# Kernel tuning notes

Measured on AMD Instinct MI355X. Metric: run time of the kernel, lower is better.

The kernel has to match this reference:

```python
import jax, jax.numpy as jnp
import numpy as np

N, E, F_IN = 100000, 1000000, 128
H, C = 4, 32
HC = H * C
D_DIR = 128
G = 250
HID, CLS = 128, 2
ALPHA = 0.5
NEG = 0.2  # LeakyReLU slope in GATv2


def setup_inputs() -> dict:
    key = jax.random.key(0)
    ks = jax.random.split(key, 16)
    p = lambda k, shape: 0.02 * jax.random.normal(k, shape, jnp.float32)
    return {
        "x": jax.random.normal(ks[0], (N, F_IN), jnp.float32),
        "edge_index": jax.random.randint(ks[1], (2, E), 0, N, dtype=jnp.int32),
        "edge_attr": jax.random.normal(ks[2], (E, 1), jnp.float32),
        "batch": jnp.sort(jax.random.randint(ks[3], (N,), 0, G, dtype=jnp.int32)),
        "dir_w_in": p(ks[4], (2, F_IN, D_DIR)),
        "dir_b_in": jnp.zeros((2, D_DIR), jnp.float32),
        "dir_w_out": p(ks[5], (2, F_IN, D_DIR)),
        "dir_b_out": jnp.zeros((2, D_DIR), jnp.float32),
        "gat_wl": p(ks[6], (F_IN, HC)),
        "gat_wr": p(ks[7], (F_IN, HC)),
        "gat_we": p(ks[8], (1, HC)),
        "gat_att": p(ks[9], (H, C)),
        "gat_b": jnp.zeros((HC,), jnp.float32),
        "w1": p(ks[10], (D_DIR + HC, HID)),
        "b1": jnp.zeros((HID,), jnp.float32),
        "w2": p(ks[11], (HID, CLS)),
        "b2": jnp.zeros((CLS,), jnp.float32),
    }


def _gcn(x, src, dst, W, b):
    # GCNConv with add_self_loops=False (forced by DirGNNConv), unit edge weights.
    deg = jnp.zeros((N,), x.dtype).at[dst].add(1.0)
    dinv = jnp.where(deg > 0, 1.0 / jnp.sqrt(jnp.maximum(deg, 1.0)), 0.0)
    norm = dinv[src] * dinv[dst]  # [E]
    h = x @ W  # [N, D]
    out = jnp.zeros((N, W.shape[1]), x.dtype).at[dst].add(norm[:, None] * h[src])
    return out + b


def _mean_pool(h, batch):
    cnt = jnp.zeros((G,), h.dtype).at[batch].add(1.0)
    s = jnp.zeros((G, h.shape[1]), h.dtype).at[batch].add(h)
    return s / jnp.maximum(cnt, 1.0)[:, None]


def _forward(x, edge_index, edge_attr, batch, dir_w_in, dir_b_in, dir_w_out, dir_b_out,
             gat_wl, gat_wr, gat_we, gat_att, gat_b, w1, b1, w2, b2):
    src, dst = edge_index[0], edge_index[1]
    # --- DirGNN branch: alpha * GCN(flipped edges) + (1-alpha) * GCN(edges), relu between ---
    h = x
    for i in range(2):
        x_in = _gcn(h, src, dst, dir_w_in[i], dir_b_in[i])
        x_out = _gcn(h, dst, src, dir_w_out[i], dir_b_out[i])
        h = jax.nn.relu(ALPHA * x_out + (1.0 - ALPHA) * x_in)
    x1 = _mean_pool(h, batch)  # [G, D_DIR]
    # --- GATv2 branch (self loops appended, edge_attr fill value 1.0) ---
    loop = jnp.arange(N, dtype=src.dtype)
    s2 = jnp.concatenate([src, loop])
    d2 = jnp.concatenate([dst, loop])
    ea = jnp.concatenate([edge_attr, jnp.ones((N, 1), edge_attr.dtype)], axis=0)
    gl = (x @ gat_wl).reshape(N, H, C)  # source transform
    gr = (x @ gat_wr).reshape(N, H, C)  # target transform
    ee = (ea @ gat_we).reshape(-1, H, C)
    e = jax.nn.leaky_relu(gl[s2] + gr[d2] + ee, NEG)  # [E+N, H, C]
    logits = jnp.einsum('ehc,hc->eh', e, gat_att)
    # segment softmax over incoming edges of each target node (self loops => nonempty)
    m = jnp.full((N, H), -jnp.inf, logits.dtype).at[d2].max(logits)
    ex = jnp.exp(logits - m[d2])
    denom = jnp.zeros((N, H), logits.dtype).at[d2].add(ex)
    att = ex / denom[d2]
    out2 = jnp.zeros((N, H, C), x.dtype).at[d2].add(att[:, :, None] * gl[s2])
    x2 = _mean_pool(out2.reshape(N, HC) + gat_b, batch)  # [G, HC]
    # --- head ---
    z = jnp.concatenate([x1, x2], axis=1)
    z = jax.nn.relu(z @ w1 + b1)
    return z @ w2 + b2  # [G, CLS]


def reference(x, edge_index, edge_attr, batch, dir_w_in, dir_b_in, dir_w_out, dir_b_out,
              gat_wl, gat_wr, gat_we, gat_att, gat_b, w1, b1, w2, b2):
    return _forward(x, edge_index, edge_attr, batch, dir_w_in, dir_b_in, dir_w_out, dir_b_out,
                    gat_wl, gat_wr, gat_we, gat_att, gat_b, w1, b1, w2, b2)
```

## Files before the change

kernel.cpp:

```cpp
#include <hip/hip_runtime.h>
#include <cstdint>

#define FDIM 128
#define PCH 64

static inline int cdiv(long long a, long long b) { return (int)((a + b - 1) / b); }

__global__ __launch_bounds__(256) void degi_kernel(const int* __restrict__ src,
                                                   const int* __restrict__ dst,
                                                   int* __restrict__ deg_in,
                                                   int* __restrict__ deg_out, int E) {
  int base = (blockIdx.x * 256 + threadIdx.x) * 2;
  if (base + 2 <= E) {
    int2 s2 = *(const int2*)(src + base);
    int2 d2 = *(const int2*)(dst + base);
    atomicAdd(&deg_in[d2.x], 1);
    atomicAdd(&deg_in[d2.y], 1);
    atomicAdd(&deg_out[s2.x], 1);
    atomicAdd(&deg_out[s2.y], 1);
  } else {
    for (int i = base; i < E; i++) {
      atomicAdd(&deg_in[dst[i]], 1);
      atomicAdd(&deg_out[src[i]], 1);
    }
  }
}

__global__ __launch_bounds__(256) void dinv2_kernel(const int* __restrict__ degs,
                                                    float* __restrict__ dinv, int n2) {
  int i = blockIdx.x * 256 + threadIdx.x;
  if (i < n2) {
    int v = degs[i];
    dinv[i] = v > 0 ? 1.0f / sqrtf((float)v) : 0.f;
  }
}

__global__ __launch_bounds__(256) void cnt_sorted(const int* __restrict__ batch,
                                                  float* __restrict__ cnt, int N, int G) {
  int g = blockIdx.x * 256 + threadIdx.x;
  if (g >= G) return;
  int lo = 0, hi = N;
  while (lo < hi) { int mid = (lo + hi) >> 1; if (batch[mid] < g) lo = mid + 1; else hi = mid; }
  int lo2 = lo, hi2 = N;
  while (lo2 < hi2) { int mid = (lo2 + hi2) >> 1; if (batch[mid] <= g) lo2 = mid + 1; else hi2 = mid; }
  cnt[g] = (float)(lo2 - lo);
}

__global__ __launch_bounds__(256) void scan1(const int* __restrict__ in, int* __restrict__ out,
                                             int* __restrict__ bsums, int n) {
  __shared__ int tmp[256];
  int t = threadIdx.x;
  int base = blockIdx.x * 1024 + t * 4;
  int a[4];
#pragma unroll
  for (int j = 0; j < 4; j++) a[j] = (base + j < n) ? in[base + j] : 0;
  int s = a[0] + a[1] + a[2] + a[3];
  tmp[t] = s;
  __syncthreads();
  for (int off = 1; off < 256; off <<= 1) {
    int v = (t >= off) ? tmp[t - off] : 0;
    __syncthreads();
    tmp[t] += v;
    __syncthreads();
  }
  int excl = tmp[t] - s;
  int run = excl;
#pragma unroll
  for (int j = 0; j < 4; j++) {
    if (base + j < n) out[base + j] = run;
    run += a[j];
  }
  if (t == 255) bsums[blockIdx.x] = tmp[255];
}

__global__ __launch_bounds__(256) void scan2(const int* __restrict__ bsums,
                                             int* __restrict__ boff, int nb) {
  __shared__ int tmp[256];
  int t = threadIdx.x;
  int s = (t < nb) ? bsums[t] : 0;
  tmp[t] = s;
  __syncthreads();
  for (int off = 1; off < 256; off <<= 1) {
    int v = (t >= off) ? tmp[t - off] : 0;
    __syncthreads();
    tmp[t] += v;
    __syncthreads();
  }
  if (t < nb) boff[t] = tmp[t] - s;
}

__global__ __launch_bounds__(256) void scan3(const int* __restrict__ scanned,
                                             const int* __restrict__ boff,
                                             int* __restrict__ rp_in, int* __restrict__ cur_in,
                                             int* __restrict__ rp_out, int* __restrict__ cur_out,
                                             int N, int E, int n2) {
  int i = blockIdx.x * 256 + threadIdx.x;
  if (i < n2) {
    int v = scanned[i] + boff[i >> 10];
    if (i < N) { rp_in[i] = v; cur_in[i] = v; }
    else { v -= E; rp_out[i - N] = v; cur_out[i - N] = v; }
  }
}

__global__ __launch_bounds__(256) void mm0_fill(const float* __restrict__ A,
                                                const float* __restrict__ W0,
                                                const float* __restrict__ W1,
                                                float* __restrict__ out0,
                                                float* __restrict__ out1, int nrows, int mmB,
                                                const int* __restrict__ src,
                                                const int* __restrict__ dst,
                                                const float* __restrict__ eattr,
                                                int* __restrict__ cur_in,
                                                int* __restrict__ cur_out,
                                                int2* __restrict__ csr_in,
                                                int* __restrict__ csr_out_dst, int E, int fillB) {
  __shared__ float As[64][128];
  __shared__ float Ws[64][64];
  int T = mmB + fillB;
  int bid = blockIdx.x;
  int tid = threadIdx.x;
  long long f0 = (long long)bid * fillB / T;
  long long f1 = (long long)(bid + 1) * fillB / T;

  if (f1 > f0) {
    int base = ((int)f0 * 256 + tid) * 4;
    if (base + 4 <= E) {
      int4 s4 = *(const int4*)(src + base);
      int4 d4 = *(const int4*)(dst + base);
      float4 e4 = *(const float4*)(eattr + base);
      int p0 = atomicAdd(&cur_in[d4.x], 1);
      int p1 = atomicAdd(&cur_in[d4.y], 1);
      int p2 = atomicAdd(&cur_in[d4.z], 1);
      int p3 = atomicAdd(&cur_in[d4.w], 1);
      int q0 = atomicAdd(&cur_out[s4.x], 1);
      int q1 = atomicAdd(&cur_out[s4.y], 1);
      int q2 = atomicAdd(&cur_out[s4.z], 1);
      int q3 = atomicAdd(&cur_out[s4.w], 1);
      csr_in[p0] = make_int2(s4.x, __float_as_int(e4.x));
      csr_in[p1] = make_int2(s4.y, __float_as_int(e4.y));
      csr_in[p2] = make_int2(s4.z, __float_as_int(e4.z));
      csr_in[p3] = make_int2(s4.w, __float_as_int(e4.w));
      csr_out_dst[q0] = d4.x;
      csr_out_dst[q1] = d4.y;
      csr_out_dst[q2] = d4.z;
      csr_out_dst[q3] = d4.w;
    } else {
      for (int i = base; i < E; i++) {
        int s = src[i], d = dst[i];
        int p = atomicAdd(&cur_in[d], 1);
        csr_in[p] = make_int2(s, __float_as_int(eattr[i]));
        int q = atomicAdd(&cur_out[s], 1);
        csr_out_dst[q] = d;
      }
    }
    return;
  }

  int mb = bid - (int)f0;
  int r0 = mb * 64;

#pragma unroll
  for (int i = 0; i < 8; i++) {
    int v = tid + 256 * i;
    int r = v >> 5, k4 = (v & 31) << 2;
    int row = r0 + r;
    float4 a;
    if (row < nrows) a = *(const float4*)(A + (size_t)row * FDIM + k4);
    else a = make_float4(0.f, 0.f, 0.f, 0.f);
    int swz = ((r >> 2) & 7) << 2;
    *(float4*)(&As[r][k4 ^ swz]) = a;
  }

  int tx = tid & 15, ty = tid >> 4;
  int rbase = ty * 4;
  int swz = (ty & 7) << 2;

  for (int p = 0; p < 4; p++) {
    const float* W = (p < 2) ? W0 : W1;
    float* out = (p < 2) ? out0 : out1;
    int cb = (p & 1) * 64;
    float acc[4][4] = {};

    for (int kh = 0; kh < 2; kh++) {
      __syncthreads();
#pragma unroll
      for (int i = 0; i < 4; i++) {
        int v = tid + 256 * i;
        int k = v >> 4, c4 = (v & 15) << 2;
        *(float4*)(&Ws[k][c4]) = *(const float4*)(W + (kh * 64 + k) * FDIM + cb + c4);
      }
      __syncthreads();

#pragma unroll 8
      for (int k = 0; k < 64; k++) {
        int kx = (kh * 64 + k) ^ swz;
        float a0 = As[rbase + 0][kx];
        float a1 = As[rbase + 1][kx];
        float a2 = As[rbase + 2][kx];
        float a3 = As[rbase + 3][kx];
        float4 w = *(float4*)(&Ws[k][tx * 4]);
        acc[0][0] += a0 * w.x; acc[0][1] += a0 * w.y; acc[0][2] += a0 * w.z; acc[0][3] += a0 * w.w;
        acc[1][0] += a1 * w.x; acc[1][1] += a1 * w.y; acc[1][2] += a1 * w.z; acc[1][3] += a1 * w.w;
        acc[2][0] += a2 * w.x; acc[2][1] += a2 * w.y; acc[2][2] += a2 * w.z; acc[2][3] += a2 * w.w;
        acc[3][0] += a3 * w.x; acc[3][1] += a3 * w.y; acc[3][2] += a3 * w.z; acc[3][3] += a3 * w.w;
      }
    }

#pragma unroll
    for (int rr = 0; rr < 4; rr++) {
      int row = r0 + rbase + rr;
      if (row < nrows) {
        float4 o = make_float4(acc[rr][0], acc[rr][1], acc[rr][2], acc[rr][3]);
        *(float4*)(out + (size_t)row * FDIM + cb + tx * 4) = o;
      }
    }
  }
}

__global__ __launch_bounds__(256) void mm128d(const float* __restrict__ A,
                                              const float* __restrict__ W0,
                                              const float* __restrict__ W1,
                                              float* __restrict__ out0,
                                              float* __restrict__ out1, int nrows) {
  __shared__ float As[64][128];
  __shared__ float Ws[64][64];
  int r0 = blockIdx.x * 64;
  int tid = threadIdx.x;

#pragma unroll
  for (int i = 0; i < 8; i++) {
    int v = tid + 256 * i;
    int r = v >> 5, k4 = (v & 31) << 2;
    int row = r0 + r;
    float4 a;
    if (row < nrows) a = *(const float4*)(A + (size_t)row * FDIM + k4);
    else a = make_float4(0.f, 0.f, 0.f, 0.f);
    int swz = ((r >> 2) & 7) << 2;
    *(float4*)(&As[r][k4 ^ swz]) = a;
  }

  int tx = tid & 15, ty = tid >> 4;
  int rbase = ty * 4;
  int swz = (ty & 7) << 2;

  for (int p = 0; p < 4; p++) {
    const float* W = (p < 2) ? W0 : W1;
    float* out = (p < 2) ? out0 : out1;
    int cb = (p & 1) * 64;
    float acc[4][4] = {};

    for (int kh = 0; kh < 2; kh++) {
      __syncthreads();
#pragma unroll
      for (int i = 0; i < 4; i++) {
        int v = tid + 256 * i;
        int k = v >> 4, c4 = (v & 15) << 2;
        *(float4*)(&Ws[k][c4]) = *(const float4*)(W + (kh * 64 + k) * FDIM + cb + c4);
      }
      __syncthreads();

#pragma unroll 8
      for (int k = 0; k < 64; k++) {
        int kx = (kh * 64 + k) ^ swz;
        float a0 = As[rbase + 0][kx];
        float a1 = As[rbase + 1][kx];
        float a2 = As[rbase + 2][kx];
        float a3 = As[rbase + 3][kx];
        float4 w = *(float4*)(&Ws[k][tx * 4]);
        acc[0][0] += a0 * w.x; acc[0][1] += a0 * w.y; acc[0][2] += a0 * w.z; acc[0][3] += a0 * w.w;
        acc[1][0] += a1 * w.x; acc[1][1] += a1 * w.y; acc[1][2] += a1 * w.z; acc[1][3] += a1 * w.w;
        acc[2][0] += a2 * w.x; acc[2][1] += a2 * w.y; acc[2][2] += a2 * w.z; acc[2][3] += a2 * w.w;
        acc[3][0] += a3 * w.x; acc[3][1] += a3 * w.y; acc[3][2] += a3 * w.z; acc[3][3] += a3 * w.w;
      }
    }

#pragma unroll
    for (int rr = 0; rr < 4; rr++) {
      int row = r0 + rbase + rr;
      if (row < nrows) {
        float4 o = make_float4(acc[rr][0], acc[rr][1], acc[rr][2], acc[rr][3]);
        *(float4*)(out + (size_t)row * FDIM + cb + tx * 4) = o;
      }
    }
  }
}

__global__ __launch_bounds__(128) void gcn_gather4(const float4* __restrict__ tin,
                                                   const float4* __restrict__ tout,
                                                   const int* __restrict__ rp_in,
                                                   const int* __restrict__ deg_in,
                                                   const int2* __restrict__ adj_in,
                                                   const int* __restrict__ rp_out,
                                                   const int* __restrict__ deg_out,
                                                   const int* __restrict__ adj_out,
                                                   const float* __restrict__ dinv_in,
                                                   const float* __restrict__ dinv_out,
                                                   const float* __restrict__ bin,
                                                   const float* __restrict__ bout,
                                                   float4* __restrict__ outp, int N) {
  int grp = threadIdx.x >> 5, lane = threadIdx.x & 31;
  int d = blockIdx.x * 4 + grp;
  if (d >= N) return;
  float wi = 0.5f * dinv_in[d], wo = 0.5f * dinv_out[d];
  float4 a0 = make_float4(0.f, 0.f, 0.f, 0.f);
  float4 a1 = a0, a2 = a0, a3 = a0;

  int p = rp_in[d], n1 = deg_in[d];
  int k = 0;
  for (; k + 4 <= n1; k += 4) {
    int s0 = adj_in[p + k].x, s1 = adj_in[p + k + 1].x, s2 = adj_in[p + k + 2].x, s3 = adj_in[p + k + 3].x;
    float w0 = wi * dinv_in[s0], w1 = wi * dinv_in[s1], w2 = wi * dinv_in[s2], w3 = wi * dinv_in[s3];
    float4 v0 = tin[(size_t)s0 * 32 + lane];
    float4 v1 = tin[(size_t)s1 * 32 + lane];
    float4 v2 = tin[(size_t)s2 * 32 + lane];
    float4 v3 = tin[(size_t)s3 * 32 + lane];
    a0.x += w0 * v0.x; a0.y += w0 * v0.y; a0.z += w0 * v0.z; a0.w += w0 * v0.w;
    a1.x += w1 * v1.x; a1.y += w1 * v1.y; a1.z += w1 * v1.z; a1.w += w1 * v1.w;
    a2.x += w2 * v2.x; a2.y += w2 * v2.y; a2.z += w2 * v2.z; a2.w += w2 * v2.w;
    a3.x += w3 * v3.x; a3.y += w3 * v3.y; a3.z += w3 * v3.z; a3.w += w3 * v3.w;
  }
  for (; k < n1; k++) {
    int s = adj_in[p + k].x;
    float w = wi * dinv_in[s];
    float4 v = tin[(size_t)s * 32 + lane];
    a0.x += w * v.x; a0.y += w * v.y; a0.z += w * v.z; a0.w += w * v.w;
  }

  int q = rp_out[d], n2 = deg_out[d];
  k = 0;
  for (; k + 4 <= n2; k += 4) {
    int s0 = adj_out[q + k], s1 = adj_out[q + k + 1], s2 = adj_out[q + k + 2], s3 = adj_out[q + k + 3];
    float w0 = wo * dinv_out[s0], w1 = wo * dinv_out[s1], w2 = wo * dinv_out[s2], w3 = wo * dinv_out[s3];
    float4 v0 = tout[(size_t)s0 * 32 + lane];
    float4 v1 = tout[(size_t)s1 * 32 + lane];
    float4 v2 = tout[(size_t)s2 * 32 + lane];
    float4 v3 = tout[(size_t)s3 * 32 + lane];
    a0.x += w0 * v0.x; a0.y += w0 * v0.y; a0.z += w0 * v0.z; a0.w += w0 * v0.w;
    a1.x += w1 * v1.x; a1.y += w1 * v1.y; a1.z += w1 * v1.z; a1.w += w1 * v1.w;
    a2.x += w2 * v2.x; a2.y += w2 * v2.y; a2.z += w2 * v2.z; a2.w += w2 * v2.w;
    a3.x += w3 * v3.x; a3.y += w3 * v3.y; a3.z += w3 * v3.z; a3.w += w3 * v3.w;
  }
  for (; k < n2; k++) {
    int s = adj_out[q + k];
    float w = wo * dinv_out[s];
    float4 v = tout[(size_t)s * 32 + lane];
    a0.x += w * v.x; a0.y += w * v.y; a0.z += w * v.z; a0.w += w * v.w;
  }

  float4 acc;
  acc.x = (a0.x + a1.x) + (a2.x + a3.x);
  acc.y = (a0.y + a1.y) + (a2.y + a3.y);
  acc.z = (a0.z + a1.z) + (a2.z + a3.z);
  acc.w = (a0.w + a1.w) + (a2.w + a3.w);

  const float4* b1 = (const float4*)bin;
  const float4* b2 = (const float4*)bout;
  float4 ba = b1[lane], bb = b2[lane];
  float4 o;
  o.x = acc.x + 0.5f * (ba.x + bb.x);
  o.y = acc.y + 0.5f * (ba.y + bb.y);
  o.z = acc.z + 0.5f * (ba.z + bb.z);
  o.w = acc.w + 0.5f * (ba.w + bb.w);
  o.x = o.x > 0.f ? o.x : 0.f;
  o.y = o.y > 0.f ? o.y : 0.f;
  o.z = o.z > 0.f ? o.z : 0.f;
  o.w = o.w > 0.f ? o.w : 0.f;
  outp[(size_t)d * 32 + lane] = o;
}

__global__ __launch_bounds__(128) void gat_fused2(const float4* __restrict__ gl,
                                                  const float4* __restrict__ gr,
                                                  const int* __restrict__ rp,
                                                  const int* __restrict__ deg,
                                                  const int2* __restrict__ adj,
                                                  const float* __restrict__ we,
                                                  const float* __restrict__ att,
                                                  const float* __restrict__ gatb,
                                                  float4* __restrict__ outp, int N) {
  int grp = threadIdx.x >> 5, lane = threadIdx.x & 31;
  int d = blockIdx.x * 4 + grp;
  if (d >= N) return;

  float4 grv = gr[(size_t)d * 32 + lane];
  float4 wev = ((const float4*)we)[lane];
  float4 atv = ((const float4*)att)[lane];

  int p = rp[d], n1 = deg[d];
  float m = -1e30f, den = 0.f;
  float4 o = make_float4(0.f, 0.f, 0.f, 0.f);

#define GAT_LOGIT(g4, ea, pv)                                                     \
  {                                                                               \
    float vx = g4.x + grv.x + (ea) * wev.x; vx = vx > 0.f ? vx : 0.2f * vx;       \
    float vy = g4.y + grv.y + (ea) * wev.y; vy = vy > 0.f ? vy : 0.2f * vy;       \
    float vz = g4.z + grv.z + (ea) * wev.z; vz = vz > 0.f ? vz : 0.2f * vz;       \
    float vw = g4.w + grv.w + (ea) * wev.w; vw = vw > 0.f ? vw : 0.2f * vw;       \
    pv = vx * atv.x + vy * atv.y + vz * atv.z + vw * atv.w;                       \
    pv += __shfl_xor(pv, 1);                                                      \
    pv += __shfl_xor(pv, 2);                                                      \
    pv += __shfl_xor(pv, 4);                                                      \
  }

#define GAT_UPDATE(g4, pv)                                                        \
  {                                                                               \
    float mn = fmaxf(m, pv);                                                      \
    float sc = expf(m - mn);                                                      \
    float w = expf(pv - mn);                                                      \
    den = den * sc + w;                                                           \
    o.x = o.x * sc + w * g4.x;                                                    \
    o.y = o.y * sc + w * g4.y;                                                    \
    o.z = o.z * sc + w * g4.z;                                                    \
    o.w = o.w * sc + w * g4.w;                                                    \
    m = mn;                                                                       \
  }

  int k = 0;
  for (; k + 2 <= n1; k += 2) {
    int2 e0 = adj[p + k], e1 = adj[p + k + 1];
    int s0 = e0.x, s1 = e1.x;
    float ea0 = __int_as_float(e0.y), ea1 = __int_as_float(e1.y);
    float4 g0 = gl[(size_t)s0 * 32 + lane];
    float4 g1 = gl[(size_t)s1 * 32 + lane];
    float pv0, pv1;
    GAT_LOGIT(g0, ea0, pv0);
    GAT_LOGIT(g1, ea1, pv1);
    GAT_UPDATE(g0, pv0);
    GAT_UPDATE(g1, pv1);
  }
  if (k < n1) {
    int2 e = adj[p + k];
    float ea = __int_as_float(e.y);
    float4 g = gl[(size_t)e.x * 32 + lane];
    float pv;
    GAT_LOGIT(g, ea, pv);
    GAT_UPDATE(g, pv);
  }
  {
    float4 g = gl[(size_t)d * 32 + lane];
    float pv;
    GAT_LOGIT(g, 1.0f, pv);
    GAT_UPDATE(g, pv);
  }
#undef GAT_LOGIT
#undef GAT_UPDATE

  float4 bb = ((const float4*)gatb)[lane];
  float4 r;
  r.x = o.x / den + bb.x;
  r.y = o.y / den + bb.y;
  r.z = o.z / den + bb.z;
  r.w = o.w / den + bb.w;
  outp[(size_t)d * 32 + lane] = r;
}

__global__ __launch_bounds__(128) void pool_kernel(const float* __restrict__ srcf,
                                                   const int* __restrict__ batch,
                                                   float* __restrict__ zb,
                                                   int colOff, int N) {
  __shared__ int sb[PCH];
  int c0 = blockIdx.x * PCH;
  int t = threadIdx.x;
  int nmax = N - c0; if (nmax > PCH) nmax = PCH;
  if (t < nmax) sb[t] = batch[c0 + t];
  __syncthreads();
  float run = 0.f;
  int gp = sb[0];
  for (int i = 0; i < nmax; i++) {
    int g = sb[i];
    if (g != gp) {
      atomicAdd(&zb[(size_t)gp * 256 + colOff + t], run);
      run = 0.f; gp = g;
    }
    run += srcf[(size_t)(c0 + i) * FDIM + t];
  }
  atomicAdd(&zb[(size_t)gp * 256 + colOff + t], run);
}

__global__ __launch_bounds__(128) void head_kernel(const float* __restrict__ zb,
                                                   const float* __restrict__ cnt,
                                                   const float* __restrict__ w1,
                                                   const float* __restrict__ b1,
                                                   const float* __restrict__ w2,
                                                   const float* __restrict__ b2,
                                                   float* __restrict__ out, int G) {
  __shared__ float z[256];
  __shared__ float y[128];
  int g = blockIdx.x, t = threadIdx.x;
  float c = cnt[g];
  float cm = c > 1.f ? c : 1.f;
  z[t]       = zb[(size_t)g * 256 + t] / cm;
  z[t + 128] = zb[(size_t)g * 256 + 128 + t] / cm;
  __syncthreads();
  float acc = b1[t];
  for (int k = 0; k < 256; k++) acc += z[k] * w1[k * 128 + t];
  y[t] = acc > 0.f ? acc : 0.f;
  __syncthreads();
  if (t < 2) {
    float o = b2[t];
    for (int j = 0; j < 128; j++) o += y[j] * w2[j * 2 + t];
    out[(size_t)g * 2 + t] = o;
  }
}

extern "C" void kernel_launch(void* const* d_in, const int* in_sizes, int n_in,
                              void* d_out, int out_size, void* d_ws, size_t ws_size,
                              hipStream_t stream) {
  const float* x     = (const float*)d_in[0];
  const int*   ei    = (const int*)d_in[1];
  const float* eattr = (const float*)d_in[2];
  const int*   batch = (const int*)d_in[3];
  const float* dwi   = (const float*)d_in[4];
  const float* dbi   = (const float*)d_in[5];
  const float* dwo   = (const float*)d_in[6];
  const float* dbo   = (const float*)d_in[7];
  const float* wl    = (const float*)d_in[8];
  const float* wr    = (const float*)d_in[9];
  const float* we    = (const float*)d_in[10];
  const float* att   = (const float*)d_in[11];
  const float* gatb  = (const float*)d_in[12];
  const float* w1    = (const float*)d_in[13];
  const float* b1    = (const float*)d_in[14];
  const float* w2    = (const float*)d_in[15];
  const float* b2    = (const float*)d_in[16];

  int N = in_sizes[0] / FDIM;
  int E = in_sizes[1] / 2;
  int G = out_size / 2;
  const int* src = ei;
  const int* dst = ei + E;

  float* ws = (float*)d_ws;
  size_t off = 0;
  float* A        = ws + off; off += (size_t)N * FDIM;
  float* B        = ws + off; off += (size_t)N * FDIM;
  float* C        = ws + off; off += (size_t)N * FDIM;
  float* dinv2    = ws + off; off += 2 * (size_t)N;
  int* deg2       = (int*)(ws + off); off += 2 * (size_t)N;
  int* rpt        = (int*)(ws + off); off += 2 * (size_t)N;
  int* rp_in      = (int*)(ws + off); off += (size_t)N;
  int* rp_out     = (int*)(ws + off); off += (size_t)N;
  int* cur_in     = (int*)(ws + off); off += (size_t)N;
  int* cur_out    = (int*)(ws + off); off += (size_t)N;
  int2* csr_in    = (int2*)(ws + off); off += 2 * (size_t)E;
  int* csr_out_dst= (int*)(ws + off); off += (size_t)E;
  int* bsums      = (int*)(ws + off); off += 256;
  int* boff       = (int*)(ws + off); off += 256;
  float* zb       = ws + off; off += (size_t)G * 256;
  float* cnt      = ws + off; off += (size_t)G;

  int* deg_in = deg2, *deg_out = deg2 + N;
  float* dinv_in = dinv2, *dinv_out = dinv2 + N;

  int n2 = 2 * N;
  int nb1 = cdiv(n2, 1024);

  hipMemsetAsync(deg2, 0, (size_t)n2 * sizeof(int), stream);
  degi_kernel<<<cdiv(E, 512), 256, 0, stream>>>(src, dst, deg_in, deg_out, E);
  dinv2_kernel<<<cdiv((long long)n2, 256), 256, 0, stream>>>(deg2, dinv2, n2);
  scan1<<<nb1, 256, 0, stream>>>(deg2, rpt, bsums, n2);
  scan2<<<1, 256, 0, stream>>>(bsums, boff, nb1);
  scan3<<<cdiv(n2, 256), 256, 0, stream>>>(rpt, boff, rp_in, cur_in, rp_out, cur_out, N, E, n2);

  hipMemsetAsync(zb, 0, (size_t)G * 256 * sizeof(float), stream);
  cnt_sorted<<<cdiv(G, 256), 256, 0, stream>>>(batch, cnt, N, G);

  int mmB = cdiv(N, 64);
  int fillB = cdiv(E, 1024);
  mm0_fill<<<mmB + fillB, 256, 0, stream>>>(x, dwi, dwo, B, C, N, mmB,
                                            src, dst, eattr, cur_in, cur_out,
                                            csr_in, csr_out_dst, E, fillB);

  gcn_gather4<<<cdiv(N, 4), 128, 0, stream>>>((const float4*)B, (const float4*)C,
                                              rp_in, deg_in, csr_in,
                                              rp_out, deg_out, csr_out_dst,
                                              dinv_in, dinv_out, dbi, dbo, (float4*)A, N);
  mm128d<<<mmB, 256, 0, stream>>>(A, dwi + 16384, dwo + 16384, B, C, N);
  gcn_gather4<<<cdiv(N, 4), 128, 0, stream>>>((const float4*)B, (const float4*)C,
                                              rp_in, deg_in, csr_in,
                                              rp_out, deg_out, csr_out_dst,
                                              dinv_in, dinv_out, dbi + 128, dbo + 128, (float4*)A, N);
  pool_kernel<<<cdiv(N, PCH), 128, 0, stream>>>(A, batch, zb, 0, N);

  mm128d<<<mmB, 256, 0, stream>>>(x, wl, wr, B, C, N);
  gat_fused2<<<cdiv(N, 4), 128, 0, stream>>>((const float4*)B, (const float4*)C,
                                             rp_in, deg_in, csr_in,
                                             we, att, gatb, (float4*)A, N);
  pool_kernel<<<cdiv(N, PCH), 128, 0, stream>>>(A, batch, zb, 128, N);

  head_kernel<<<G, 128, 0, stream>>>(zb, cnt, w1, b1, w2, b2, (float*)d_out, G);
}
```

Baseline: 1.082 ms.

## Fuse GAT matmul with degree count and fuse pooling into gather kernels

Moves the GAT input projection into the degree-counting kernel so the two run concurrently, using a fourth workspace buffer when space allows. GAT aggregation and the second GCN gather now atomically add their node results straight into the per-graph pooled sums, which removes the separate pool kernels and the round trip of the node feature matrix. The fused pooling relies on float atomics into a small per-graph array, which may contend and changes summation order. A fallback path keeps a three-buffer schedule when the workspace is too small.

After: 1.477 ms. 1.36x slower.

```diff
diff --git a/kernel.cpp b/kernel.cpp
--- a/kernel.cpp
+++ b/kernel.cpp
@@ -102,7 +102,257 @@
   }
 }
 
-__global__ __launch_bounds__(256) void mm0_fill(const float* __restrict__ A,
+
+__device__ __forceinline__ float4 gcn_node_val(int d, int lane,
+    const float4* __restrict__ tin, const float4* __restrict__ tout,
+    const int* __restrict__ rp_in, const int* __restrict__ deg_in, const int2* __restrict__ adj_in,
+    const int* __restrict__ rp_out, const int* __restrict__ deg_out, const int* __restrict__ adj_out,
+    const float* __restrict__ dinv_in, const float* __restrict__ dinv_out,
+    const float* __restrict__ bin, const float* __restrict__ bout) {
+  float wi = 0.5f * dinv_in[d], wo = 0.5f * dinv_out[d];
+  float4 a0 = make_float4(0.f, 0.f, 0.f, 0.f);
+  float4 a1 = a0, a2 = a0, a3 = a0;
+
+  int p = rp_in[d], n1 = deg_in[d];
+  int k = 0;
+  for (; k + 4 <= n1; k += 4) {
+    int s0 = adj_in[p + k].x, s1 = adj_in[p + k + 1].x, s2 = adj_in[p + k + 2].x, s3 = adj_in[p + k + 3].x;
+    float w0 = wi * dinv_in[s0], w1 = wi * dinv_in[s1], w2 = wi * dinv_in[s2], w3 = wi * dinv_in[s3];
+    float4 v0 = tin[(size_t)s0 * 32 + lane];
+    float4 v1 = tin[(size_t)s1 * 32 + lane];
+    float4 v2 = tin[(size_t)s2 * 32 + lane];
+    float4 v3 = tin[(size_t)s3 * 32 + lane];
+    a0.x += w0 * v0.x; a0.y += w0 * v0.y; a0.z += w0 * v0.z; a0.w += w0 * v0.w;
+    a1.x += w1 * v1.x; a1.y += w1 * v1.y; a1.z += w1 * v1.z; a1.w += w1 * v1.w;
+    a2.x += w2 * v2.x; a2.y += w2 * v2.y; a2.z += w2 * v2.z; a2.w += w2 * v2.w;
+    a3.x += w3 * v3.x; a3.y += w3 * v3.y; a3.z += w3 * v3.z; a3.w += w3 * v3.w;
+  }
+  for (; k < n1; k++) {
+    int s = adj_in[p + k].x;
+    float w = wi * dinv_in[s];
+    float4 v = tin[(size_t)s * 32 + lane];
+    a0.x += w * v.x; a0.y += w * v.y; a0.z += w * v.z; a0.w += w * v.w;
+  }
+
+  int q = rp_out[d], n2 = deg_out[d];
+  k = 0;
+  for (; k + 4 <= n2; k += 4) {
+    int s0 = adj_out[q + k], s1 = adj_out[q + k + 1], s2 = adj_out[q + k + 2], s3 = adj_out[q + k + 3];
+    float w0 = wo * dinv_out[s0], w1 = wo * dinv_out[s1], w2 = wo * dinv_out[s2], w3 = wo * dinv_out[s3];
+    float4 v0 = tout[(size_t)s0 * 32 + lane];
+    float4 v1 = tout[(size_t)s1 * 32 + lane];
+    float4 v2 = tout[(size_t)s2 * 32 + lane];
+    float4 v3 = tout[(size_t)s3 * 32 + lane];
+    a0.x += w0 * v0.x; a0.y += w0 * v0.y; a0.z += w0 * v0.z; a0.w += w0 * v0.w;
+    a1.x += w1 * v1.x; a1.y += w1 * v1.y; a1.z += w1 * v1.z; a1.w += w1 * v1.w;
+    a2.x += w2 * v2.x; a2.y += w2 * v2.y; a2.z += w2 * v2.z; a2.w += w2 * v2.w;
+    a3.x += w3 * v3.x; a3.y += w3 * v3.y; a3.z += w3 * v3.z; a3.w += w3 * v3.w;
+  }
+  for (; k < n2; k++) {
+    int s = adj_out[q + k];
+    float w = wo * dinv_out[s];
+    float4 v = tout[(size_t)s * 32 + lane];
+    a0.x += w * v.x; a0.y += w * v.y; a0.z += w * v.z; a0.w += w * v.w;
+  }
+
+  float4 acc;
+  acc.x = (a0.x + a1.x) + (a2.x + a3.x);
+  acc.y = (a0.y + a1.y) + (a2.y + a3.y);
+  acc.z = (a0.z + a1.z) + (a2.z + a3.z);
+  acc.w = (a0.w + a1.w) + (a2.w + a3.w);
+
+  float4 ba = ((const float4*)bin)[lane], bb = ((const float4*)bout)[lane];
+  float4 o;
+  o.x = acc.x + 0.5f * (ba.x + bb.x);
+  o.y = acc.y + 0.5f * (ba.y + bb.y);
+  o.z = acc.z + 0.5f * (ba.z + bb.z);
+  o.w = acc.w + 0.5f * (ba.w + bb.w);
+  o.x = o.x > 0.f ? o.x : 0.f;
+  o.y = o.y > 0.f ? o.y : 0.f;
+  o.z = o.z > 0.f ? o.z : 0.f;
+  o.w = o.w > 0.f ? o.w : 0.f;
+  return o;
+}
+
+__device__ __forceinline__ float4 gat_node_val(int d, int lane,
+    const float4* __restrict__ gl, const float4* __restrict__ gr,
+    const int* __restrict__ rp, const int* __restrict__ deg, const int2* __restrict__ adj,
+    const float* __restrict__ we, const float* __restrict__ att,
+    const float* __restrict__ gatb) {
+  float4 grv = gr[(size_t)d * 32 + lane];
+  float4 wev = ((const float4*)we)[lane];
+  float4 atv = ((const float4*)att)[lane];
+
+  int p = rp[d], n1 = deg[d];
+  float m = -1e30f, den = 0.f;
+  float4 o = make_float4(0.f, 0.f, 0.f, 0.f);
+
+#define GAT_LOGIT(g4, ea, pv)                                                     \
+  {                                                                               \
+    float vx = g4.x + grv.x + (ea) * wev.x; vx = vx > 0.f ? vx : 0.2f * vx;       \
+    float vy = g4.y + grv.y + (ea) * wev.y; vy = vy > 0.f ? vy : 0.2f * vy;       \
+    float vz = g4.z + grv.z + (ea) * wev.z; vz = vz > 0.f ? vz : 0.2f * vz;       \
+    float vw = g4.w + grv.w + (ea) * wev.w; vw = vw > 0.f ? vw : 0.2f * vw;       \
+    pv = vx * atv.x + vy * atv.y + vz * atv.z + vw * atv.w;                       \
+    pv += __shfl_xor(pv, 1);                                                      \
+    pv += __shfl_xor(pv, 2);                                                      \
+    pv += __shfl_xor(pv, 4);                                                      \
+  }
+
+#define GAT_UPDATE(g4, pv)                                                        \
+  {                                                                               \
+    float mn = fmaxf(m, pv);                                                      \
+    float sc = expf(m - mn);                                                      \
+    float w = expf(pv - mn);                                                      \
+    den = den * sc + w;                                                           \
+    o.x = o.x * sc + w * g4.x;                                                    \
+    o.y = o.y * sc + w * g4.y;                                                    \
+    o.z = o.z * sc + w * g4.z;                                                    \
+    o.w = o.w * sc + w * g4.w;                                                    \
+    m = mn;                                                                       \
+  }
+
+  int k = 0;
+  for (; k + 2 <= n1; k += 2) {
+    int2 e0 = adj[p + k], e1 = adj[p + k + 1];
+    float ea0 = __int_as_float(e0.y), ea1 = __int_as_float(e1.y);
+    float4 g0 = gl[(size_t)e0.x * 32 + lane];
+    float4 g1 = gl[(size_t)e1.x * 32 + lane];
+    float pv0, pv1;
+    GAT_LOGIT(g0, ea0, pv0);
+    GAT_LOGIT(g1, ea1, pv1);
+    GAT_UPDATE(g0, pv0);
+    GAT_UPDATE(g1, pv1);
+  }
+  if (k < n1) {
+    int2 e = adj[p + k];
+    float ea = __int_as_float(e.y);
+    float4 g = gl[(size_t)e.x * 32 + lane];
+    float pv;
+    GAT_LOGIT(g, ea, pv);
+    GAT_UPDATE(g, pv);
+  }
+  {
+    float4 g = gl[(size_t)d * 32 + lane];
+    float pv;
+    GAT_LOGIT(g, 1.0f, pv);
+    GAT_UPDATE(g, pv);
+  }
+#undef GAT_LOGIT
+#undef GAT_UPDATE
+
+  float4 bb = ((const float4*)gatb)[lane];
+  float4 r;
+  r.x = o.x / den + bb.x;
+  r.y = o.y / den + bb.y;
+  r.z = o.z / den + bb.z;
+  r.w = o.w / den + bb.w;
+  return r;
+}
+
+__device__ __forceinline__ void mm64_dual(const float* __restrict__ A,
+                                          const float* __restrict__ W0,
+                                          const float* __restrict__ W1,
+                                          float* __restrict__ out0,
+                                          float* __restrict__ out1,
+                                          int nrows, int r0, int tid,
+                                          float (*As)[128], float (*Ws)[64]) {
+#pragma unroll
+  for (int i = 0; i < 8; i++) {
+    int v = tid + 256 * i;
+    int r = v >> 5, k4 = (v & 31) << 2;
+    int row = r0 + r;
+    float4 a;
+    if (row < nrows) a = *(const float4*)(A + (size_t)row * FDIM + k4);
+    else a = make_float4(0.f, 0.f, 0.f, 0.f);
+    int swz = ((r >> 2) & 7) << 2;
+    *(float4*)(&As[r][k4 ^ swz]) = a;
+  }
+
+  int tx = tid & 15, ty = tid >> 4;
+  int rbase = ty * 4;
+  int swz = (ty & 7) << 2;
+
+  for (int p = 0; p < 4; p++) {
+    const float* W = (p < 2) ? W0 : W1;
+    float* out = (p < 2) ? out0 : out1;
+    int cb = (p & 1) * 64;
+    float acc[4][4] = {};
+
+    for (int kh = 0; kh < 2; kh++) {
+      __syncthreads();
+#pragma unroll
+      for (int i = 0; i < 4; i++) {
+        int v = tid + 256 * i;
+        int k = v >> 4, c4 = (v & 15) << 2;
+        *(float4*)(&Ws[k][c4]) = *(const float4*)(W + (kh * 64 + k) * FDIM + cb + c4);
+      }
+      __syncthreads();
+
+#pragma unroll 8
+      for (int k = 0; k < 64; k++) {
+        int kx = (kh * 64 + k) ^ swz;
+        float a0 = As[rbase + 0][kx];
+        float a1 = As[rbase + 1][kx];
+        float a2 = As[rbase + 2][kx];
+        float a3 = As[rbase + 3][kx];
+        float4 w = *(float4*)(&Ws[k][tx * 4]);
+        acc[0][0] += a0 * w.x; acc[0][1] += a0 * w.y; acc[0][2] += a0 * w.z; acc[0][3] += a0 * w.w;
+        acc[1][0] += a1 * w.x; acc[1][1] += a1 * w.y; acc[1][2] += a1 * w.z; acc[1][3] += a1 * w.w;
+        acc[2][0] += a2 * w.x; acc[2][1] += a2 * w.y; acc[2][2] += a2 * w.z; acc[2][3] += a2 * w.w;
+        acc[3][0] += a3 * w.x; acc[3][1] += a3 * w.y; acc[3][2] += a3 * w.z; acc[3][3] += a3 * w.w;
+      }
+    }
+
+#pragma unroll
+    for (int rr = 0; rr < 4; rr++) {
+      int row = r0 + rbase + rr;
+      if (row < nrows) {
+        float4 o = make_float4(acc[rr][0], acc[rr][1], acc[rr][2], acc[rr][3]);
+        *(float4*)(out + (size_t)row * FDIM + cb + tx * 4) = o;
+      }
+    }
+  }
+}
+
+
+__global__ __launch_bounds__(256) void mmgat_degi(const float* __restrict__ x,
+                                                  const float* __restrict__ wl,
+                                                  const float* __restrict__ wr,
+                                                  float* __restrict__ B,
+                                                  float* __restrict__ C, int N, int mmB,
+                                                  const int* __restrict__ src,
+                                                  const int* __restrict__ dst,
+                                                  int* __restrict__ deg_in,
+                                                  int* __restrict__ deg_out, int E, int degB) {
+  __shared__ float As[64][128];
+  __shared__ float Ws[64][64];
+  int T = mmB + degB;
+  int bid = blockIdx.x, tid = threadIdx.x;
+  long long f0 = (long long)bid * degB / T;
+  long long f1 = (long long)(bid + 1) * degB / T;
+  if (f1 > f0) {
+    int base = ((int)f0 * 256 + tid) * 2;
+    if (base + 2 <= E) {
+      int2 s2 = *(const int2*)(src + base);
+      int2 d2 = *(const int2*)(dst + base);
+      atomicAdd(&deg_in[d2.x], 1);
+      atomicAdd(&deg_in[d2.y], 1);
+      atomicAdd(&deg_out[s2.x], 1);
+      atomicAdd(&deg_out[s2.y], 1);
+    } else {
+      for (int i = base; i < E; i++) {
+        atomicAdd(&deg_in[dst[i]], 1);
+        atomicAdd(&deg_out[src[i]], 1);
+      }
+    }
+    return;
+  }
+  int mb = bid - (int)f0;
+  mm64_dual(x, wl, wr, B, C, N, mb * 64, tid, As, Ws);
+}
+
+__global__ __launch_bounds__(256) void mm0_fill(const float* __restrict__ x,
                                                 const float* __restrict__ W0,
                                                 const float* __restrict__ W1,
                                                 float* __restrict__ out0,
@@ -157,132 +407,29 @@
   }
 
   int mb = bid - (int)f0;
-  int r0 = mb * 64;
-
-#pragma unroll
-  for (int i = 0; i < 8; i++) {
-    int v = tid + 256 * i;
-    int r = v >> 5, k4 = (v & 31) << 2;
-    int row = r0 + r;
-    float4 a;
-    if (row < nrows) a = *(const float4*)(A + (size_t)row * FDIM + k4);
-    else a = make_float4(0.f, 0.f, 0.f, 0.f);
-    int swz = ((r >> 2) & 7) << 2;
-    *(float4*)(&As[r][k4 ^ swz]) = a;
-  }
-
-  int tx = tid & 15, ty = tid >> 4;
-  int rbase = ty * 4;
-  int swz = (ty & 7) << 2;
-
-  for (int p = 0; p < 4; p++) {
-    const float* W = (p < 2) ? W0 : W1;
-    float* out = (p < 2) ? out0 : out1;
-    int cb = (p & 1) * 64;
-    float acc[4][4] = {};
-
-    for (int kh = 0; kh < 2; kh++) {
-      __syncthreads();
-#pragma unroll
-      for (int i = 0; i < 4; i++) {
-        int v = tid + 256 * i;
-        int k = v >> 4, c4 = (v & 15) << 2;
-        *(float4*)(&Ws[k][c4]) = *(const float4*)(W + (kh * 64 + k) * FDIM + cb + c4);
-      }
-      __syncthreads();
-
-#pragma unroll 8
-      for (int k = 0; k < 64; k++) {
-        int kx = (kh * 64 + k) ^ swz;
-        float a0 = As[rbase + 0][kx];
-        float a1 = As[rbase + 1][kx];
-        float a2 = As[rbase + 2][kx];
-        float a3 = As[rbase + 3][kx];
-        float4 w = *(float4*)(&Ws[k][tx * 4]);
-        acc[0][0] += a0 * w.x; acc[0][1] += a0 * w.y; acc[0][2] += a0 * w.z; acc[0][3] += a0 * w.w;
-        acc[1][0] += a1 * w.x; acc[1][1] += a1 * w.y; acc[1][2] += a1 * w.z; acc[1][3] += a1 * w.w;
-        acc[2][0] += a2 * w.x; acc[2][1] += a2 * w.y; acc[2][2] += a2 * w.z; acc[2][3] += a2 * w.w;
-        acc[3][0] += a3 * w.x; acc[3][1] += a3 * w.y; acc[3][2] += a3 * w.z; acc[3][3] += a3 * w.w;
-      }
-    }
-
-#pragma unroll
-    for (int rr = 0; rr < 4; rr++) {
-      int row = r0 + rbase + rr;
-      if (row < nrows) {
-        float4 o = make_float4(acc[rr][0], acc[rr][1], acc[rr][2], acc[rr][3]);
-        *(float4*)(out + (size_t)row * FDIM + cb + tx * 4) = o;
-      }
-    }
-  }
-}
-
-__global__ __launch_bounds__(256) void mm128d(const float* __restrict__ A,
-                                              const float* __restrict__ W0,
-                                              const float* __restrict__ W1,
-                                              float* __restrict__ out0,
-                                              float* __restrict__ out1, int nrows) {
-  __shared__ float As[64][128];
-  __shared__ float Ws[64][64];
-  int r0 = blockIdx.x * 64;
-  int tid = threadIdx.x;
-
-#pragma unroll
-  for (int i = 0; i < 8; i++) {
-    int v = tid + 256 * i;
-    int r = v >> 5, k4 = (v & 31) << 2;
-    int row = r0 + r;
-    float4 a;
-    if (row < nrows) a = *(const float4*)(A + (size_t)row * FDIM + k4);
-    else a = make_float4(0.f, 0.f, 0.f, 0.f);
-    int swz = ((r >> 2) & 7) << 2;
-    *(float4*)(&As[r][k4 ^ swz]) = a;
-  }
-
-  int tx = tid & 15, ty = tid >> 4;
-  int rbase = ty * 4;
-  int swz = (ty & 7) << 2;
-
-  for (int p = 0; p < 4; p++) {
-    const float* W = (p < 2) ? W0 : W1;
-    float* out = (p < 2) ? out0 : out1;
-    int cb = (p & 1) * 64;
-    float acc[4][4] = {};
-
-    for (int kh = 0; kh < 2; kh++) {
-      __syncthreads();
-#pragma unroll
-      for (int i = 0; i < 4; i++) {
-        int v = tid + 256 * i;
-        int k = v >> 4, c4 = (v & 15) << 2;
-        *(float4*)(&Ws[k][c4]) = *(const float4*)(W + (kh * 64 + k) * FDIM + cb + c4);
-      }
-      __syncthreads();
-
-#pragma unroll 8
-      for (int k = 0; k < 64; k++) {
-        int kx = (kh * 64 + k) ^ swz;
-        float a0 = As[rbase + 0][kx];
-        float a1 = As[rbase + 1][kx];
-        float a2 = As[rbase + 2][kx];
-        float a3 = As[rbase + 3][kx];
-        float4 w = *(float4*)(&Ws[k][tx * 4]);
-        acc[0][0] += a0 * w.x; acc[0][1] += a0 * w.y; acc[0][2] += a0 * w.z; acc[0][3] += a0 * w.w;
-        acc[1][0] += a1 * w.x; acc[1][1] += a1 * w.y; acc[1][2] += a1 * w.z; acc[1][3] += a1 * w.w;
-        acc[2][0] += a2 * w.x; acc[2][1] += a2 * w.y; acc[2][2] += a2 * w.z; acc[2][3] += a2 * w.w;
-        acc[3][0] += a3 * w.x; acc[3][1] += a3 * w.y; acc[3][2] += a3 * w.z; acc[3][3] += a3 * w.w;
-      }
-    }
-
-#pragma unroll
-    for (int rr = 0; rr < 4; rr++) {
-      int row = r0 + rbase + rr;
-      if (row < nrows) {
-        float4 o = make_float4(acc[rr][0], acc[rr][1], acc[rr][2], acc[rr][3]);
-        *(float4*)(out + (size_t)row * FDIM + cb + tx * 4) = o;
-      }
-    }
-  }
+  mm64_dual(x, W0, W1, out0, out1, nrows, mb * 64, tid, As, Ws);
+}
+
+__global__ __launch_bounds__(128) void gat_pool(const float4* __restrict__ gl,
+                                                const float4* __restrict__ gr,
+                                                const int* __restrict__ rp,
+                                                const int* __restrict__ deg,
+                                                const int2* __restrict__ adj,
+                                                const float* __restrict__ we,
+                                                const float* __restrict__ att,
+                                                const float* __restrict__ gatb,
+                                                const int* __restrict__ batch,
+                                                float* __restrict__ zb, int N) {
+  int grp = threadIdx.x >> 5, lane = threadIdx.x & 31;
+  int d = blockIdx.x * 4 + grp;
+  if (d >= N) return;
+  float4 r = gat_node_val(d, lane, gl, gr, rp, deg, adj, we, att, gatb);
+  int g = batch[d];
+  float* dstp = &zb[(size_t)g * 256 + 128 + lane * 4];
+  atomicAdd(dstp + 0, r.x);
+  atomicAdd(dstp + 1, r.y);
+  atomicAdd(dstp + 2, r.z);
+  atomicAdd(dstp + 3, r.w);
 }
 
 __global__ __launch_bounds__(128) void gcn_gather4(const float4* __restrict__ tin,
@@ -301,71 +448,39 @@
   int grp = threadIdx.x >> 5, lane = threadIdx.x & 31;
   int d = blockIdx.x * 4 + grp;
   if (d >= N) return;
-  float wi = 0.5f * dinv_in[d], wo = 0.5f * dinv_out[d];
-  float4 a0 = make_float4(0.f, 0.f, 0.f, 0.f);
-  float4 a1 = a0, a2 = a0, a3 = a0;
-
-  int p = rp_in[d], n1 = deg_in[d];
-  int k = 0;
-  for (; k + 4 <= n1; k += 4) {
-    int s0 = adj_in[p + k].x, s1 = adj_in[p + k + 1].x, s2 = adj_in[p + k + 2].x, s3 = adj_in[p + k + 3].x;
-    float w0 = wi * dinv_in[s0], w1 = wi * dinv_in[s1], w2 = wi * dinv_in[s2], w3 = wi * dinv_in[s3];
-    float4 v0 = tin[(size_t)s0 * 32 + lane];
-    float4 v1 = tin[(size_t)s1 * 32 + lane];
-    float4 v2 = tin[(size_t)s2 * 32 + lane];
-    float4 v3 = tin[(size_t)s3 * 32 + lane];
-    a0.x += w0 * v0.x; a0.y += w0 * v0.y; a0.z += w0 * v0.z; a0.w += w0 * v0.w;
-    a1.x += w1 * v1.x; a1.y += w1 * v1.y; a1.z += w1 * v1.z; a1.w += w1 * v1.w;
-    a2.x += w2 * v2.x; a2.y += w2 * v2.y; a2.z += w2 * v2.z; a2.w += w2 * v2.w;
-    a3.x += w3 * v3.x; a3.y += w3 * v3.y; a3.z += w3 * v3.z; a3.w += w3 * v3.w;
-  }
-  for (; k < n1; k++) {
-    int s = adj_in[p + k].x;
-    float w = wi * dinv_in[s];
-    float4 v = tin[(size_t)s * 32 + lane];
-    a0.x += w * v.x; a0.y += w * v.y; a0.z += w * v.z; a0.w += w * v.w;
-  }
-
-  int q = rp_out[d], n2 = deg_out[d];
-  k = 0;
-  for (; k + 4 <= n2; k += 4) {
-    int s0 = adj_out[q + k], s1 = adj_out[q + k + 1], s2 = adj_out[q + k + 2], s3 = adj_out[q + k + 3];
-    float w0 = wo * dinv_out[s0], w1 = wo * dinv_out[s1], w2 = wo * dinv_out[s2], w3 = wo * dinv_out[s3];
-    float4 v0 = tout[(size_t)s0 * 32 + lane];
-    float4 v1 = tout[(size_t)s1 * 32 + lane];
-    float4 v2 = tout[(size_t)s2 * 32 + lane];
-    float4 v3 = tout[(size_t)s3 * 32 + lane];
-    a0.x += w0 * v0.x; a0.y += w0 * v0.y; a0.z += w0 * v0.z; a0.w += w0 * v0.w;
-    a1.x += w1 * v1.x; a1.y += w1 * v1.y; a1.z += w1 * v1.z; a1.w += w1 * v1.w;
-    a2.x += w2 * v2.x; a2.y += w2 * v2.y; a2.z += w2 * v2.z; a2.w += w2 * v2.w;
-    a3.x += w3 * v3.x; a3.y += w3 * v3.y; a3.z += w3 * v3.z; a3.w += w3 * v3.w;
-  }
-  for (; k < n2; k++) {
-    int s = adj_out[q + k];
-    float w = wo * dinv_out[s];
-    float4 v = tout[(size_t)s * 32 + lane];
-    a0.x += w * v.x; a0.y += w * v.y; a0.z += w * v.z; a0.w += w * v.w;
-  }
-
-  float4 acc;
-  acc.x = (a0.x + a1.x) + (a2.x + a3.x);
-  acc.y = (a0.y + a1.y) + (a2.y + a3.y);
-  acc.z = (a0.z + a1.z) + (a2.z + a3.z);
-  acc.w = (a0.w + a1.w) + (a2.w + a3.w);
-
-  const float4* b1 = (const float4*)bin;
-  const float4* b2 = (const float4*)bout;
-  float4 ba = b1[lane], bb = b2[lane];
-  float4 o;
-  o.x = acc.x + 0.5f * (ba.x + bb.x);
-  o.y = acc.y + 0.5f * (ba.y + bb.y);
-  o.z = acc.z + 0.5f * (ba.z + bb.z);
-  o.w = acc.w + 0.5f * (ba.w + bb.w);
-  o.x = o.x > 0.f ? o.x : 0.f;
-  o.y = o.y > 0.f ? o.y : 0.f;
-  o.z = o.z > 0.f ? o.z : 0.f;
-  o.w = o.w > 0.f ? o.w : 0.f;
+  float4 o = gcn_node_val(d, lane, tin, tout, rp_in, deg_in, adj_in,
+                          rp_out, deg_out, adj_out, dinv_in, dinv_out, bin, bout);
   outp[(size_t)d * 32 + lane] = o;
+}
+
+__global__ __launch_bounds__(128) void gcn_gather_pool(
+    const float4* __restrict__ tin, const float4* __restrict__ tout,
+    const int* __restrict__ rp_in, const int* __restrict__ deg_in, const int2* __restrict__ adj_in,
+    const int* __restrict__ rp_out, const int* __restrict__ deg_out, const int* __restrict__ adj_out,
+    const float* __restrict__ dinv_in, const float* __restrict__ dinv_out,
+    const float* __restrict__ bin, const float* __restrict__ bout,
+    const int* __restrict__ batch, float* __restrict__ zb, int N) {
+  int grp = threadIdx.x >> 5, lane = threadIdx.x & 31;
+  int d = blockIdx.x * 4 + grp;
+  if (d >= N) return;
+  float4 o = gcn_node_val(d, lane, tin, tout, rp_in, deg_in, adj_in,
+                          rp_out, deg_out, adj_out, dinv_in, dinv_out, bin, bout);
+  int g = batch[d];
+  float* dstp = &zb[(size_t)g * 256 + lane * 4];
+  atomicAdd(dstp + 0, o.x);
+  atomicAdd(dstp + 1, o.y);
+  atomicAdd(dstp + 2, o.z);
+  atomicAdd(dstp + 3, o.w);
+}
+
+__global__ __launch_bounds__(256) void mm128d(const float* __restrict__ A,
+                                              const float* __restrict__ W0,
+                                              const float* __restrict__ W1,
+                                              float* __restrict__ out0,
+                                              float* __restrict__ out1, int nrows) {
+  __shared__ float As[64][128];
+  __shared__ float Ws[64][64];
+  mm64_dual(A, W0, W1, out0, out1, nrows, blockIdx.x * 64, threadIdx.x, As, Ws);
 }
 
 __global__ __launch_bounds__(128) void gat_fused2(const float4* __restrict__ gl,
@@ -380,76 +495,7 @@
   int grp = threadIdx.x >> 5, lane = threadIdx.x & 31;
   int d = blockIdx.x * 4 + grp;
   if (d >= N) return;
-
-  float4 grv = gr[(size_t)d * 32 + lane];
-  float4 wev = ((const float4*)we)[lane];
-  float4 atv = ((const float4*)att)[lane];
-
-  int p = rp[d], n1 = deg[d];
-  float m = -1e30f, den = 0.f;
-  float4 o = make_float4(0.f, 0.f, 0.f, 0.f);
-
-#define GAT_LOGIT(g4, ea, pv)                                                     \
-  {                                                                               \
-    float vx = g4.x + grv.x + (ea) * wev.x; vx = vx > 0.f ? vx : 0.2f * vx;       \
-    float vy = g4.y + grv.y + (ea) * wev.y; vy = vy > 0.f ? vy : 0.2f * vy;       \
-    float vz = g4.z + grv.z + (ea) * wev.z; vz = vz > 0.f ? vz : 0.2f * vz;       \
-    float vw = g4.w + grv.w + (ea) * wev.w; vw = vw > 0.f ? vw : 0.2f * vw;       \
-    pv = vx * atv.x + vy * atv.y + vz * atv.z + vw * atv.w;                       \
-    pv += __shfl_xor(pv, 1);                                                      \
-    pv += __shfl_xor(pv, 2);                                                      \
-    pv += __shfl_xor(pv, 4);                                                      \
-  }
-
-#define GAT_UPDATE(g4, pv)                                                        \
-  {                                                                               \
-    float mn = fmaxf(m, pv);                                                      \
-    float sc = expf(m - mn);                                                      \
-    float w = expf(pv - mn);                                                      \
-    den = den * sc + w;                                                           \
-    o.x = o.x * sc + w * g4.x;                                                    \
-    o.y = o.y * sc + w * g4.y;                                                    \
-    o.z = o.z * sc + w * g4.z;                                                    \
-    o.w = o.w * sc + w * g4.w;                                                    \
-    m = mn;                                                                       \
-  }
-
-  int k = 0;
-  for (; k + 2 <= n1; k += 2) {
-    int2 e0 = adj[p + k], e1 = adj[p + k + 1];
-    int s0 = e0.x, s1 = e1.x;
-    float ea0 = __int_as_float(e0.y), ea1 = __int_as_float(e1.y);
-    float4 g0 = gl[(size_t)s0 * 32 + lane];
-    float4 g1 = gl[(size_t)s1 * 32 + lane];
-    float pv0, pv1;
-    GAT_LOGIT(g0, ea0, pv0);
-    GAT_LOGIT(g1, ea1, pv1);
-    GAT_UPDATE(g0, pv0);
-    GAT_UPDATE(g1, pv1);
-  }
-  if (k < n1) {
-    int2 e = adj[p + k];
-    float ea = __int_as_float(e.y);
-    float4 g = gl[(size_t)e.x * 32 + lane];
-    float pv;
-    GAT_LOGIT(g, ea, pv);
-    GAT_UPDATE(g, pv);
-  }
-  {
-    float4 g = gl[(size_t)d * 32 + lane];
-    float pv;
-    GAT_LOGIT(g, 1.0f, pv);
-    GAT_UPDATE(g, pv);
-  }
-#undef GAT_LOGIT
-#undef GAT_UPDATE
-
-  float4 bb = ((const float4*)gatb)[lane];
-  float4 r;
-  r.x = o.x / den + bb.x;
-  r.y = o.y / den + bb.y;
-  r.z = o.z / den + bb.z;
-  r.w = o.w / den + bb.w;
+  float4 r = gat_node_val(d, lane, gl, gr, rp, deg, adj, we, att, gatb);
   outp[(size_t)d * 32 + lane] = r;
 }
 
@@ -529,11 +575,18 @@
   const int* src = ei;
   const int* dst = ei + E;
 
+  size_t nf = (size_t)N * FDIM;
+  size_t fixed = 10 * (size_t)N + 3 * (size_t)E + 512 + (size_t)G * 257;
+  bool main_path = ((4 * nf + fixed) * sizeof(float)) <= ws_size;
+  int nbuf = main_path ? 4 : 3;
+
   float* ws = (float*)d_ws;
   size_t off = 0;
-  float* A        = ws + off; off += (size_t)N * FDIM;
-  float* B        = ws + off; off += (size_t)N * FDIM;
-  float* C        = ws + off; off += (size_t)N * FDIM;
+  float* A = ws + off; off += nf;
+  float* B = ws + off; off += nf;
+  float* C = ws + off; off += nf;
+  float* D = nullptr;
+  if (nbuf == 4) { D = ws + off; off += nf; }
   float* dinv2    = ws + off; off += 2 * (size_t)N;
   int* deg2       = (int*)(ws + off); off += 2 * (size_t)N;
   int* rpt        = (int*)(ws + off); off += 2 * (size_t)N;
@@ -553,39 +606,62 @@
 
   int n2 = 2 * N;
   int nb1 = cdiv(n2, 1024);
-
-  hipMemsetAsync(deg2, 0, (size_t)n2 * sizeof(int), stream);
-  degi_kernel<<<cdiv(E, 512), 256, 0, stream>>>(src, dst, deg_in, deg_out, E);
-  dinv2_kernel<<<cdiv((long long)n2, 256), 256, 0, stream>>>(deg2, dinv2, n2);
-  scan1<<<nb1, 256, 0, stream>>>(deg2, rpt, bsums, n2);
-  scan2<<<1, 256, 0, stream>>>(bsums, boff, nb1);
-  scan3<<<cdiv(n2, 256), 256, 0, stream>>>(rpt, boff, rp_in, cur_in, rp_out, cur_out, N, E, n2);
-
-  hipMemsetAsync(zb, 0, (size_t)G * 256 * sizeof(float), stream);
-  cnt_sorted<<<cdiv(G, 256), 256, 0, stream>>>(batch, cnt, N, G);
-
   int mmB = cdiv(N, 64);
   int fillB = cdiv(E, 1024);
-  mm0_fill<<<mmB + fillB, 256, 0, stream>>>(x, dwi, dwo, B, C, N, mmB,
-                                            src, dst, eattr, cur_in, cur_out,
-                                            csr_in, csr_out_dst, E, fillB);
-
-  gcn_gather4<<<cdiv(N, 4), 128, 0, stream>>>((const float4*)B, (const float4*)C,
-                                              rp_in, deg_in, csr_in,
-                                              rp_out, deg_out, csr_out_dst,
-                                              dinv_in, dinv_out, dbi, dbo, (float4*)A, N);
-  mm128d<<<mmB, 256, 0, stream>>>(A, dwi + 16384, dwo + 16384, B, C, N);
-  gcn_gather4<<<cdiv(N, 4), 128, 0, stream>>>((const float4*)B, (const float4*)C,
-                                              rp_in, deg_in, csr_in,
-                                              rp_out, deg_out, csr_out_dst,
-                                              dinv_in, dinv_out, dbi + 128, dbo + 128, (float4*)A, N);
-  pool_kernel<<<cdiv(N, PCH), 128, 0, stream>>>(A, batch, zb, 0, N);
-
-  mm128d<<<mmB, 256, 0, stream>>>(x, wl, wr, B, C, N);
-  gat_fused2<<<cdiv(N, 4), 128, 0, stream>>>((const float4*)B, (const float4*)C,
+  int degB = cdiv(E, 512);
+
+  hipMemsetAsync(deg2, 0, (size_t)n2 * sizeof(int), stream);
+  hipMemsetAsync(zb, 0, (size_t)G * 256 * sizeof(float), stream);
+
+  if (main_path) {
+    mmgat_degi<<<mmB + degB, 256, 0, stream>>>(x, wl, wr, B, C, N, mmB,
+                                               src, dst, deg_in, deg_out, E, degB);
+    dinv2_kernel<<<cdiv((long long)n2, 256), 256, 0, stream>>>(deg2, dinv2, n2);
+    scan1<<<nb1, 256, 0, stream>>>(deg2, rpt, bsums, n2);
+    scan2<<<1, 256, 0, stream>>>(bsums, boff, nb1);
+    scan3<<<cdiv(n2, 256), 256, 0, stream>>>(rpt, boff, rp_in, cur_in, rp_out, cur_out, N, E, n2);
+    cnt_sorted<<<cdiv(G, 256), 256, 0, stream>>>(batch, cnt, N, G);
+    mm0_fill<<<mmB + fillB, 256, 0, stream>>>(x, dwi, dwo, A, D, N, mmB,
+                                              src, dst, eattr, cur_in, cur_out,
+                                              csr_in, csr_out_dst, E, fillB);
+    gat_pool<<<cdiv(N, 4), 128, 0, stream>>>((const float4*)B, (const float4*)C,
                                              rp_in, deg_in, csr_in,
-                                             we, att, gatb, (float4*)A, N);
-  pool_kernel<<<cdiv(N, PCH), 128, 0, stream>>>(A, batch, zb, 128, N);
+                                             we, att, gatb, batch, zb, N);
+    gcn_gather4<<<cdiv(N, 4), 128, 0, stream>>>((const float4*)A, (const float4*)D,
+                                                rp_in, deg_in, csr_in,
+                                                rp_out, deg_out, csr_out_dst,
+                                                dinv_in, dinv_out, dbi, dbo, (float4*)B, N);
+    mm128d<<<mmB, 256, 0, stream>>>(B, dwi + 16384, dwo + 16384, C, D, N);
+    gcn_gather_pool<<<cdiv(N, 4), 128, 0, stream>>>((const float4*)C, (const float4*)D,
+                                                    rp_in, deg_in, csr_in,
+                                                    rp_out, deg_out, csr_out_dst,
+                                                    dinv_in, dinv_out, dbi + 128, dbo + 128,
+                                                    batch, zb, N);
+  } else {
+    degi_kernel<<<degB, 256, 0, stream>>>(src, dst, deg_in, deg_out, E);
+    dinv2_kernel<<<cdiv((long long)n2, 256), 256, 0, stream>>>(deg2, dinv2, n2);
+    scan1<<<nb1, 256, 0, stream>>>(deg2, rpt, bsums, n2);
+    scan2<<<1, 256, 0, stream>>>(bsums, boff, nb1);
+    scan3<<<cdiv(n2, 256), 256, 0, stream>>>(rpt, boff, rp_in, cur_in, rp_out, cur_out, N, E, n2);
+    cnt_sorted<<<cdiv(G, 256), 256, 0, stream>>>(batch, cnt, N, G);
+    mm0_fill<<<mmB + fillB, 256, 0, stream>>>(x, dwi, dwo, B, C, N, mmB,
+                                              src, dst, eattr, cur_in, cur_out,
+                                              csr_in, csr_out_dst, E, fillB);
+    gcn_gather4<<<cdiv(N, 4), 128, 0, stream>>>((const float4*)B, (const float4*)C,
+                                                rp_in, deg_in, csr_in,
+                                                rp_out, deg_out, csr_out_dst,
+                                                dinv_in, dinv_out, dbi, dbo, (float4*)A, N);
+    mm128d<<<mmB, 256, 0, stream>>>(A, dwi + 16384, dwo + 16384, B, C, N);
+    gcn_gather_pool<<<cdiv(N, 4), 128, 0, stream>>>((const float4*)B, (const float4*)C,
+                                                    rp_in, deg_in, csr_in,
+                                                    rp_out, deg_out, csr_out_dst,
+                                                    dinv_in, dinv_out, dbi + 128, dbo + 128,
+                                                    batch, zb, N);
+    mm128d<<<mmB, 256, 0, stream>>>(x, wl, wr, B, C, N);
+    gat_pool<<<cdiv(N, 4), 128, 0, stream>>>((const float4*)B, (const float4*)C,
+                                             rp_in, deg_in, csr_in,
+                                             we, att, gatb, batch, zb, N);
+  }
 
   head_kernel<<<G, 128, 0, stream>>>(zb, cnt, w1, b1, w2, b2, (float*)d_out, G);
 }
```
